# Optimization experiments

Hardware: AMD Instinct MI355X
Metric: run time of the kernel (lower is better)

Reference implementation:

```python
import jax, jax.numpy as jnp
import numpy as np
import math

D_MODEL = 1024
NUM_HEADS = 16
HEAD_DIM = D_MODEL // NUM_HEADS


def setup_inputs() -> dict:
    key = jax.random.key(0)
    ks = jax.random.split(key, 9)
    B, S = 2, 2048
    scale = 1.0 / math.sqrt(D_MODEL)
    x = jax.random.normal(ks[0], (B, S, D_MODEL), dtype=jnp.float32)
    # torch nn.Linear params: weight [out, in], bias [out]
    Wq = jax.random.normal(ks[1], (D_MODEL, D_MODEL), dtype=jnp.float32) * scale
    bq = jax.random.normal(ks[2], (D_MODEL,), dtype=jnp.float32) * scale
    Wk = jax.random.normal(ks[3], (D_MODEL, D_MODEL), dtype=jnp.float32) * scale
    bk = jax.random.normal(ks[4], (D_MODEL,), dtype=jnp.float32) * scale
    Wv = jax.random.normal(ks[5], (D_MODEL, D_MODEL), dtype=jnp.float32) * scale
    bv = jax.random.normal(ks[6], (D_MODEL,), dtype=jnp.float32) * scale
    Wo = jax.random.normal(ks[7], (D_MODEL, D_MODEL), dtype=jnp.float32) * scale
    bo = jax.random.normal(ks[8], (D_MODEL,), dtype=jnp.float32) * scale
    return {"x": x, "Wq": Wq, "bq": bq, "Wk": Wk, "bk": bk,
            "Wv": Wv, "bv": bv, "Wo": Wo, "bo": bo}


def reference(x, Wq, bq, Wk, bk, Wv, bv, Wo, bo):
    B, S, _ = x.shape
    H, Dh = NUM_HEADS, HEAD_DIM

    def proj(W, b):
        # torch Linear: x @ W.T + b -> [B,S,D] -> [B,H,S,Dh]
        y = jnp.einsum('bsd,ed->bse', x, W) + b
        return y.reshape(B, S, H, Dh).transpose(0, 2, 1, 3)

    Q = proj(Wq, bq)
    K = proj(Wk, bk)
    V = proj(Wv, bv)

    # scores [B,H,S,S], causal mask with -inf, then scale by 1/sqrt(head_dim)
    scores = jnp.einsum('bhqd,bhkd->bhqk', Q, K)
    causal = jnp.tril(jnp.ones((S, S), dtype=bool))
    scores = jnp.where(causal, scores, -jnp.inf)
    A = jax.nn.softmax(scores / math.sqrt(Dh), axis=-1)

    O = jnp.einsum('bhqk,bhkd->bhqd', A, V)  # [B,H,S,Dh]
    O = O.transpose(0, 2, 1, 3).reshape(B, S, H * Dh)
    return jnp.einsum('bsd,ed->bse', O, Wo) + bo
```

## Files before the change

### kernel.cpp

```cpp
#include <hip/hip_runtime.h>


typedef _Float16 f16x8 __attribute__((ext_vector_type(8)));
typedef _Float16 f16x4 __attribute__((ext_vector_type(4)));
typedef _Float16 f16x2 __attribute__((ext_vector_type(2)));
typedef float f32x4 __attribute__((ext_vector_type(4)));

#define S_  2048
#define DM  1024
#define NH  16
#define DH  64

__device__ __forceinline__ void gload_lds16(const void* g, void* s) {
  __builtin_amdgcn_global_load_lds(
      (const __attribute__((address_space(1))) void*)g,
      (__attribute__((address_space(3))) void*)s, 16, 0, 0);
}

__device__ __forceinline__ f16x2 pkrtz(float a, float b) {
  return __builtin_bit_cast(f16x2, __builtin_amdgcn_cvt_pkrtz(a, b));
}


__global__ void cvt_all_kernel(const float* __restrict__ x,
                               const float* __restrict__ w0,
                               const float* __restrict__ w1,
                               const float* __restrict__ w2,
                               const float* __restrict__ w3,
                               _Float16* __restrict__ xb,
                               _Float16* __restrict__ wb) {
  const int bid = blockIdx.x;
  const float* src;
  _Float16* dst;
  int idx;
  if (bid < 4096) {
    src = x; dst = xb; idx = bid * 256 + threadIdx.x;
  } else {
    const int j = bid - 4096;
    const int y = j >> 10;
    src = (y == 0) ? w0 : (y == 1) ? w1 : (y == 2) ? w2 : w3;
    dst = wb + (size_t)y * (DM * DM);
    idx = (j & 1023) * 256 + threadIdx.x;
  }
  const float4 v = ((const float4*)src)[idx];
  f16x4 h;
  h[0] = (_Float16)v.x; h[1] = (_Float16)v.y;
  h[2] = (_Float16)v.z; h[3] = (_Float16)v.w;
  ((f16x4*)dst)[idx] = h;
}


__global__ __launch_bounds__(256, 2) void gemm_qkv_kernel(
    const _Float16* __restrict__ xb, const _Float16* __restrict__ wb,
    const float* __restrict__ bq, const float* __restrict__ bk,
    const float* __restrict__ bv, _Float16* __restrict__ qkv)
{
  __shared__ _Float16 As[2][128 * 32];
  __shared__ _Float16 Ws[2][128 * 32];
  const int z = blockIdx.z;
  const _Float16* W = wb + (size_t)z * (DM * DM);
  const float* bias = (z == 0) ? bq : ((z == 1) ? bk : bv);
  _Float16* out = qkv + (size_t)z * 4194304;

  const f32x4 z4 = {0.f, 0.f, 0.f, 0.f};
  f32x4 acc[4][4];
#pragma unroll
  for (int mi = 0; mi < 4; ++mi)
#pragma unroll
    for (int ni = 0; ni < 4; ++ni) acc[mi][ni] = z4;

  const int m0 = blockIdx.y * 128, n0 = blockIdx.x * 128;
  const int t = threadIdx.x;
  const int w = t >> 6, l = t & 63;
  const int quad = l >> 4, ln = l & 15;
  const int wm = (w >> 1) << 6, wn = (w & 1) << 6;
  const int srow = l >> 2, scol = (l & 3) << 3;

  for (int k0 = 0; k0 < DM; k0 += 64) {
#pragma unroll
    for (int h = 0; h < 2; ++h)
#pragma unroll
      for (int i = 0; i < 2; ++i) {
        const int ra = w * 32 + i * 16;
        gload_lds16(&xb[(size_t)(m0 + ra + srow) * DM + k0 + h * 32 + scol],
                    &As[h][ra * 32]);
        gload_lds16(&W[(size_t)(n0 + ra + srow) * DM + k0 + h * 32 + scol],
                    &Ws[h][ra * 32]);
      }
    __syncthreads();

#pragma unroll
    for (int h = 0; h < 2; ++h) {
      f16x8 af[4], bf[4];
#pragma unroll
      for (int mi = 0; mi < 4; ++mi)
        af[mi] = *(const f16x8*)&As[h][(wm + mi * 16 + ln) * 32 + quad * 8];
#pragma unroll
      for (int ni = 0; ni < 4; ++ni)
        bf[ni] = *(const f16x8*)&Ws[h][(wn + ni * 16 + ln) * 32 + quad * 8];
#pragma unroll
      for (int mi = 0; mi < 4; ++mi)
#pragma unroll
        for (int ni = 0; ni < 4; ++ni)
          acc[mi][ni] = __builtin_amdgcn_mfma_f32_16x16x32_f16(
              af[mi], bf[ni], acc[mi][ni], 0, 0, 0);
    }
    __syncthreads();
  }

  const float scale = (z == 0) ? 0.18033688f : 1.0f;

#pragma unroll
  for (int ni = 0; ni < 4; ++ni) {
    const int c = n0 + wn + ni * 16 + ln;
    const float bias_c = bias[c];
    const int h = c >> 6, d = c & 63;
#pragma unroll
    for (int mi = 0; mi < 4; ++mi) {
      const int mb = m0 + wm + mi * 16 + quad * 4;
#pragma unroll
      for (int r = 0; r < 4; ++r) {
        const int mg = mb + r;
        const int b = mg >> 11, s = mg & 2047;
        const int bh = b * NH + h;
        const float v = (acc[mi][ni][r] + bias_c) * scale;
        size_t idx;
        if (z == 2)
          idx = (size_t)bh * 131072 + (s >> 5) * 2048 + (d >> 4) * 512 +
                ((s >> 3) & 3) * 128 + (d & 15) * 8 + (s & 7);
        else
          idx = (size_t)bh * 131072 + (s >> 4) * 1024 + (d >> 5) * 512 +
                ((d >> 3) & 3) * 128 + (s & 15) * 8 + (d & 7);
        out[idx] = (_Float16)v;
      }
    }
  }
}


__global__ __launch_bounds__(256, 2) void gemm_out_kernel(
    const _Float16* __restrict__ ob, const _Float16* __restrict__ wo,
    const float* __restrict__ bo, float* __restrict__ out)
{
  __shared__ _Float16 As[2][128 * 32];
  __shared__ _Float16 Ws[2][64 * 32];
  const f32x4 z4 = {0.f, 0.f, 0.f, 0.f};
  f32x4 acc[2][4];
#pragma unroll
  for (int mi = 0; mi < 2; ++mi)
#pragma unroll
    for (int ni = 0; ni < 4; ++ni) acc[mi][ni] = z4;

  const int m0 = blockIdx.y * 128, n0 = blockIdx.x * 64;
  const int t = threadIdx.x;
  const int w = t >> 6, l = t & 63;
  const int quad = l >> 4, ln = l & 15;
  const int srow = l >> 2, scol = (l & 3) << 3;

  for (int k0 = 0; k0 < DM; k0 += 64) {
#pragma unroll
    for (int h = 0; h < 2; ++h) {
#pragma unroll
      for (int i = 0; i < 2; ++i) {
        const int ra = w * 32 + i * 16;
        gload_lds16(&ob[(size_t)(m0 + ra + srow) * DM + k0 + h * 32 + scol],
                    &As[h][ra * 32]);
      }
      gload_lds16(&wo[(size_t)(n0 + w * 16 + srow) * DM + k0 + h * 32 + scol],
                  &Ws[h][w * 16 * 32]);
    }
    __syncthreads();

#pragma unroll
    for (int h = 0; h < 2; ++h) {
      f16x8 af[2], bf[4];
#pragma unroll
      for (int mi = 0; mi < 2; ++mi)
        af[mi] = *(const f16x8*)&As[h][(w * 32 + mi * 16 + ln) * 32 + quad * 8];
#pragma unroll
      for (int ni = 0; ni < 4; ++ni)
        bf[ni] = *(const f16x8*)&Ws[h][(ni * 16 + ln) * 32 + quad * 8];
#pragma unroll
      for (int mi = 0; mi < 2; ++mi)
#pragma unroll
        for (int ni = 0; ni < 4; ++ni)
          acc[mi][ni] = __builtin_amdgcn_mfma_f32_16x16x32_f16(
              af[mi], bf[ni], acc[mi][ni], 0, 0, 0);
    }
    __syncthreads();
  }

#pragma unroll
  for (int ni = 0; ni < 4; ++ni) {
    const int c = n0 + ni * 16 + ln;
    const float bias_c = bo[c];
#pragma unroll
    for (int mi = 0; mi < 2; ++mi) {
      const int mb = m0 + w * 32 + mi * 16 + quad * 4;
#pragma unroll
      for (int r = 0; r < 4; ++r)
        out[(size_t)(mb + r) * DM + c] = acc[mi][ni][r] + bias_c;
    }
  }
}


template <bool DIAG>
__device__ __forceinline__ void tile16(
    const _Float16* __restrict__ kb_, const _Float16* __restrict__ vb_,
    int t, const f16x8 (&qf)[2], f32x4 (&oacc)[4], float& l_i,
    _Float16* Ps, int quad, int ln, int l, int h)
{
  const f32x4 z4 = {0.f, 0.f, 0.f, 0.f};
  f16x8 kv[4];

#pragma unroll
  for (int ii = 0; ii < 4; ++ii)
    kv[ii] = *(const f16x8*)(kb_ + (size_t)(t * 4 + ii) * 512 + l * 8);

  f32x4 sacc[2];
  sacc[0] = z4; sacc[1] = z4;
#pragma unroll
  for (int ks = 0; ks < 2; ++ks)
#pragma unroll
    for (int mi = 0; mi < 2; ++mi)
      sacc[mi] = __builtin_amdgcn_mfma_f32_16x16x32_f16(
          kv[mi * 2 + ks], qf[ks], sacc[mi], 0, 0, 0);

#pragma unroll
  for (int ii = 0; ii < 4; ++ii)
    kv[ii] = *(const f16x8*)(vb_ + (size_t)(t * 4 + ii) * 512 + l * 8);

  float rs = 0.f;
#pragma unroll
  for (int mi = 0; mi < 2; ++mi) {
    float p[4];
#pragma unroll
    for (int r = 0; r < 4; ++r) {
      p[r] = __builtin_amdgcn_exp2f(sacc[mi][r]);
      if (DIAG && (mi * 16 + quad * 4 + r > h * 16 + ln)) p[r] = 0.f;
      rs += p[r];
    }
    const f16x2 lo = pkrtz(p[0], p[1]);
    const f16x2 hi = pkrtz(p[2], p[3]);
    const f16x4 pk = __builtin_shufflevector(lo, hi, 0, 1, 2, 3);
    const int slot = ((mi * 4 + quad) + 2 * ln) & 15;
    *(f16x4*)&Ps[ln * 64 + slot * 4] = pk;
  }
  l_i += rs;

  const int slot2 = ((quad * 2) + 2 * ln) & 15;
  const f16x8 pb = *(const f16x8*)&Ps[ln * 64 + slot2 * 4];

#pragma unroll
  for (int di = 0; di < 4; ++di)
    oacc[di] = __builtin_amdgcn_mfma_f32_16x16x32_f16(
        kv[di], pb, oacc[di], 0, 0, 0);
}

__global__ __launch_bounds__(256, 6) void attn_kernel(
    const _Float16* __restrict__ QF, const _Float16* __restrict__ KF,
    const _Float16* __restrict__ VF, _Float16* __restrict__ Ob)
{
  __shared__ _Float16 Ps[4 * 16 * 64];
  __shared__ float mrgO[2][1024];
  __shared__ float mrgL[2][64];

  const int i = blockIdx.x;
  const int bh = i & 31;
  const int a = 63 - (i >> 5);

  const int tid = threadIdx.x;
  const int w = tid >> 6, l = tid & 63;
  const int quad = l >> 4, ln = l & 15;
  const int h = w >> 1;
  const int e = w & 1;

  const _Float16* qb_ = QF + (size_t)bh * 131072;
  const _Float16* kb_ = KF + (size_t)bh * 131072;
  const _Float16* vb_ = VF + (size_t)bh * 131072;
  _Float16* psw = Ps + w * (16 * 64);
  const int bidx = bh >> 4, hh = bh & 15;

  f16x8 qf[2];
#pragma unroll
  for (int ks = 0; ks < 2; ++ks)
    qf[ks] = *(const f16x8*)
        (qb_ + (size_t)((a * 2 + h) * 2 + ks) * 512 + l * 8);

  const f32x4 z4 = {0.f, 0.f, 0.f, 0.f};
  f32x4 oacc[4];
#pragma unroll
  for (int di = 0; di < 4; ++di) oacc[di] = z4;
  float l_i = 0.f;

  int t = e;
  for (; t < a; t += 2)
    tile16<false>(kb_, vb_, t, qf, oacc, l_i, psw, quad, ln, l, h);
  if (t == a)
    tile16<true>(kb_, vb_, t, qf, oacc, l_i, psw, quad, ln, l, h);

  if (e) {
#pragma unroll
    for (int di = 0; di < 4; ++di)
      *(f32x4*)&mrgO[h][di * 256 + l * 4] = oacc[di];
    mrgL[h][l] = l_i;
  }
  __syncthreads();
  if (!e) {
#pragma unroll
    for (int di = 0; di < 4; ++di)
      oacc[di] += *(const f32x4*)&mrgO[h][di * 256 + l * 4];
    l_i += mrgL[h][l];
    l_i += __shfl_xor(l_i, 16);
    l_i += __shfl_xor(l_i, 32);
    const float inv = 1.0f / l_i;

    const int q = a * 32 + h * 16 + ln;
    _Float16* orow = Ob + (size_t)(bidx * S_ + q) * DM + hh * DH + quad * 4;
#pragma unroll
    for (int di = 0; di < 4; ++di) {
      f16x4 o4;
#pragma unroll
      for (int r = 0; r < 4; ++r)
        o4[r] = (_Float16)(oacc[di][r] * inv);
      *(f16x4*)(orow + di * 16) = o4;
    }
  }
}


extern "C" void kernel_launch(void* const* d_in, const int* in_sizes, int n_in,
                              void* d_out, int out_size, void* d_ws, size_t ws_size,
                              hipStream_t stream) {
  (void)in_sizes; (void)n_in; (void)out_size; (void)ws_size;
  const float* x  = (const float*)d_in[0];
  const float* Wq = (const float*)d_in[1];
  const float* bq = (const float*)d_in[2];
  const float* Wk = (const float*)d_in[3];
  const float* bk = (const float*)d_in[4];
  const float* Wv = (const float*)d_in[5];
  const float* bv = (const float*)d_in[6];
  const float* Wo = (const float*)d_in[7];
  const float* bo = (const float*)d_in[8];

  char* ws = (char*)d_ws;
  _Float16* xb  = (_Float16*)(ws);
  _Float16* wb  = (_Float16*)(ws + (8u << 20));
  _Float16* qkv = (_Float16*)(ws + (16u << 20));
  _Float16* ob  = (_Float16*)(ws + (40u << 20));

  cvt_all_kernel<<<dim3(8192), dim3(256), 0, stream>>>(x, Wq, Wk, Wv, Wo, xb, wb);
  gemm_qkv_kernel<<<dim3(8, 32, 3), dim3(256), 0, stream>>>(xb, wb, bq, bk, bv, qkv);
  attn_kernel<<<dim3(2048), dim3(256), 0, stream>>>(
      qkv, qkv + 4194304, qkv + 2 * 4194304, ob);
  gemm_out_kernel<<<dim3(16, 32), dim3(256), 0, stream>>>(
      ob, wb + (size_t)3 * DM * DM, bo, (float*)d_out);
}
```

Measured before the change: 183.0 us.

## Share K/V tiles across waves via double-buffered LDS in attention

The attention kernel now gives each block 64 query rows (four waves, 16 rows each) instead of 32 rows split over two key-parity waves. K and V tiles are streamed into double-buffered LDS with global_load_lds and shared by all four waves, replacing per-wave global loads and the cross-wave merge of partial outputs. The grid is halved. This cuts redundant K/V global traffic but adds two barriers per tile, and waves with earlier diagonals sit idle on later tiles.

```diff
diff --git a/kernel.cpp b/kernel.cpp
--- a/kernel.cpp
+++ b/kernel.cpp
@@ -206,17 +206,17 @@
 
 
 template <bool DIAG>
-__device__ __forceinline__ void tile16(
-    const _Float16* __restrict__ kb_, const _Float16* __restrict__ vb_,
-    int t, const f16x8 (&qf)[2], f32x4 (&oacc)[4], float& l_i,
-    _Float16* Ps, int quad, int ln, int l, int h)
+__device__ __forceinline__ void tile_lds(
+    const _Float16* __restrict__ Kls, const _Float16* __restrict__ Vls,
+    const f16x8 (&qf)[2], f32x4 (&oacc)[4], float& l_i,
+    _Float16* Ps, int quad, int ln, int l, int hq)
 {
   const f32x4 z4 = {0.f, 0.f, 0.f, 0.f};
   f16x8 kv[4];
 
 #pragma unroll
   for (int ii = 0; ii < 4; ++ii)
-    kv[ii] = *(const f16x8*)(kb_ + (size_t)(t * 4 + ii) * 512 + l * 8);
+    kv[ii] = *(const f16x8*)&Kls[ii * 512 + l * 8];
 
   f32x4 sacc[2];
   sacc[0] = z4; sacc[1] = z4;
@@ -229,7 +229,7 @@
 
 #pragma unroll
   for (int ii = 0; ii < 4; ++ii)
-    kv[ii] = *(const f16x8*)(vb_ + (size_t)(t * 4 + ii) * 512 + l * 8);
+    kv[ii] = *(const f16x8*)&Vls[ii * 512 + l * 8];
 
   float rs = 0.f;
 #pragma unroll
@@ -238,7 +238,7 @@
 #pragma unroll
     for (int r = 0; r < 4; ++r) {
       p[r] = __builtin_amdgcn_exp2f(sacc[mi][r]);
-      if (DIAG && (mi * 16 + quad * 4 + r > h * 16 + ln)) p[r] = 0.f;
+      if (DIAG && (mi * 16 + quad * 4 + r > hq + ln)) p[r] = 0.f;
       rs += p[r];
     }
     const f16x2 lo = pkrtz(p[0], p[1]);
@@ -262,31 +262,31 @@
     const _Float16* __restrict__ QF, const _Float16* __restrict__ KF,
     const _Float16* __restrict__ VF, _Float16* __restrict__ Ob)
 {
+  __shared__ _Float16 KVs[2][2][2048];
   __shared__ _Float16 Ps[4 * 16 * 64];
-  __shared__ float mrgO[2][1024];
-  __shared__ float mrgL[2][64];
 
   const int i = blockIdx.x;
   const int bh = i & 31;
-  const int a = 63 - (i >> 5);
+  const int b  = 31 - (i >> 5);
+  const int T  = 2 * b + 2;
 
   const int tid = threadIdx.x;
   const int w = tid >> 6, l = tid & 63;
   const int quad = l >> 4, ln = l & 15;
-  const int h = w >> 1;
-  const int e = w & 1;
+  const int hq = (w & 1) << 4;
+  const int Dw = 2 * b + (w >> 1);
 
   const _Float16* qb_ = QF + (size_t)bh * 131072;
   const _Float16* kb_ = KF + (size_t)bh * 131072;
   const _Float16* vb_ = VF + (size_t)bh * 131072;
-  _Float16* psw = Ps + w * (16 * 64);
+  _Float16* psw = Ps + w * 1024;
   const int bidx = bh >> 4, hh = bh & 15;
 
   f16x8 qf[2];
 #pragma unroll
   for (int ks = 0; ks < 2; ++ks)
     qf[ks] = *(const f16x8*)
-        (qb_ + (size_t)((a * 2 + h) * 2 + ks) * 512 + l * 8);
+        (qb_ + (size_t)((4 * b + w) * 2 + ks) * 512 + l * 8);
 
   const f32x4 z4 = {0.f, 0.f, 0.f, 0.f};
   f32x4 oacc[4];
@@ -294,38 +294,45 @@
   for (int di = 0; di < 4; ++di) oacc[di] = z4;
   float l_i = 0.f;
 
-  int t = e;
-  for (; t < a; t += 2)
-    tile16<false>(kb_, vb_, t, qf, oacc, l_i, psw, quad, ln, l, h);
-  if (t == a)
-    tile16<true>(kb_, vb_, t, qf, oacc, l_i, psw, quad, ln, l, h);
-
-  if (e) {
-#pragma unroll
-    for (int di = 0; di < 4; ++di)
-      *(f32x4*)&mrgO[h][di * 256 + l * 4] = oacc[di];
-    mrgL[h][l] = l_i;
-  }
-  __syncthreads();
-  if (!e) {
-#pragma unroll
-    for (int di = 0; di < 4; ++di)
-      oacc[di] += *(const f32x4*)&mrgO[h][di * 256 + l * 4];
-    l_i += mrgL[h][l];
-    l_i += __shfl_xor(l_i, 16);
-    l_i += __shfl_xor(l_i, 32);
-    const float inv = 1.0f / l_i;
-
-    const int q = a * 32 + h * 16 + ln;
-    _Float16* orow = Ob + (size_t)(bidx * S_ + q) * DM + hh * DH + quad * 4;
-#pragma unroll
-    for (int di = 0; di < 4; ++di) {
-      f16x4 o4;
-#pragma unroll
-      for (int r = 0; r < 4; ++r)
-        o4[r] = (_Float16)(oacc[di][r] * inv);
-      *(f16x4*)(orow + di * 16) = o4;
-    }
+  gload_lds16(&kb_[(size_t)w * 512 + l * 8], &KVs[0][0][w * 512]);
+  gload_lds16(&vb_[(size_t)w * 512 + l * 8], &KVs[0][1][w * 512]);
+
+  for (int t = 0; t < T; ++t) {
+    const int cur = t & 1;
+    if (t + 1 < T) {
+      gload_lds16(&kb_[(size_t)(t + 1) * 2048 + w * 512 + l * 8],
+                  &KVs[cur ^ 1][0][w * 512]);
+      gload_lds16(&vb_[(size_t)(t + 1) * 2048 + w * 512 + l * 8],
+                  &KVs[cur ^ 1][1][w * 512]);
+      asm volatile("s_waitcnt vmcnt(2)" ::: "memory");
+    } else {
+      asm volatile("s_waitcnt vmcnt(0)" ::: "memory");
+    }
+    __builtin_amdgcn_s_barrier();
+    __builtin_amdgcn_sched_barrier(0);
+    if (t < Dw)
+      tile_lds<false>(&KVs[cur][0][0], &KVs[cur][1][0], qf, oacc, l_i,
+                      psw, quad, ln, l, hq);
+    else if (t == Dw)
+      tile_lds<true>(&KVs[cur][0][0], &KVs[cur][1][0], qf, oacc, l_i,
+                     psw, quad, ln, l, hq);
+    __builtin_amdgcn_sched_barrier(0);
+    __builtin_amdgcn_s_barrier();
+  }
+
+  l_i += __shfl_xor(l_i, 16);
+  l_i += __shfl_xor(l_i, 32);
+  const float inv = 1.0f / l_i;
+
+  const int q = b * 64 + w * 16 + ln;
+  _Float16* orow = Ob + (size_t)(bidx * S_ + q) * DM + hh * DH + quad * 4;
+#pragma unroll
+  for (int di = 0; di < 4; ++di) {
+    f16x4 o4;
+#pragma unroll
+    for (int r = 0; r < 4; ++r)
+      o4[r] = (_Float16)(oacc[di][r] * inv);
+    *(f16x4*)(orow + di * 16) = o4;
   }
 }
 
@@ -352,7 +359,7 @@
 
   cvt_all_kernel<<<dim3(8192), dim3(256), 0, stream>>>(x, Wq, Wk, Wv, Wo, xb, wb);
   gemm_qkv_kernel<<<dim3(8, 32, 3), dim3(256), 0, stream>>>(xb, wb, bq, bk, bv, qkv);
-  attn_kernel<<<dim3(2048), dim3(256), 0, stream>>>(
+  attn_kernel<<<dim3(1024), dim3(256), 0, stream>>>(
       qkv, qkv + 4194304, qkv + 2 * 4194304, ob);
   gemm_out_kernel<<<dim3(16, 32), dim3(256), 0, stream>>>(
       ob, wb + (size_t)3 * DM * DM, bo, (float*)d_out);
```

Result: no change. 186.3 us (+1.8%).

## Process 64 query rows per attention wave to reuse K/V loads

Applied to the files above, without the earlier changes.

The attention kernel now has each wave handle four 16-row query sub-tiles over a 32-key tile, so every K and V fragment loaded from global memory is reused across 64 query rows instead of 16. Blocks shrink to two waves that split the key tiles and merge their partial sums in shared memory, and the grid halves to 1024 blocks. The diagonal tiles are handled with per-sub-tile masking modes. This cuts redundant K/V traffic but raises register use (launch bounds drop to 3 waves-per-EU hint) and lowers the total wave count, which risks lower occupancy and worse load balance.

```diff
diff --git a/kernel.cpp b/kernel.cpp
--- a/kernel.cpp
+++ b/kernel.cpp
@@ -205,126 +205,142 @@
 }
 
 
-template <bool DIAG>
-__device__ __forceinline__ void tile16(
+template <int MODE>
+__device__ __forceinline__ void tile64(
     const _Float16* __restrict__ kb_, const _Float16* __restrict__ vb_,
-    int t, const f16x8 (&qf)[2], f32x4 (&oacc)[4], float& l_i,
-    _Float16* Ps, int quad, int ln, int l, int h)
+    int t, const f16x8 (&qf)[4][2], f32x4 (&oacc)[4][4], float (&l_i)[4],
+    _Float16* Ps, int quad, int ln, int l)
 {
+  f16x8 kr[4], vr[4];
+#pragma unroll
+  for (int ii = 0; ii < 4; ++ii)
+    kr[ii] = *(const f16x8*)(kb_ + (size_t)t * 2048 + ii * 512 + l * 8);
+#pragma unroll
+  for (int ii = 0; ii < 4; ++ii)
+    vr[ii] = *(const f16x8*)(vb_ + (size_t)t * 2048 + ii * 512 + l * 8);
+
   const f32x4 z4 = {0.f, 0.f, 0.f, 0.f};
-  f16x8 kv[4];
-
-#pragma unroll
-  for (int ii = 0; ii < 4; ++ii)
-    kv[ii] = *(const f16x8*)(kb_ + (size_t)(t * 4 + ii) * 512 + l * 8);
-
-  f32x4 sacc[2];
-  sacc[0] = z4; sacc[1] = z4;
-#pragma unroll
-  for (int ks = 0; ks < 2; ++ks)
-#pragma unroll
-    for (int mi = 0; mi < 2; ++mi)
-      sacc[mi] = __builtin_amdgcn_mfma_f32_16x16x32_f16(
-          kv[mi * 2 + ks], qf[ks], sacc[mi], 0, 0, 0);
-
-#pragma unroll
-  for (int ii = 0; ii < 4; ++ii)
-    kv[ii] = *(const f16x8*)(vb_ + (size_t)(t * 4 + ii) * 512 + l * 8);
-
-  float rs = 0.f;
-#pragma unroll
-  for (int mi = 0; mi < 2; ++mi) {
-    float p[4];
-#pragma unroll
-    for (int r = 0; r < 4; ++r) {
-      p[r] = __builtin_amdgcn_exp2f(sacc[mi][r]);
-      if (DIAG && (mi * 16 + quad * 4 + r > h * 16 + ln)) p[r] = 0.f;
-      rs += p[r];
-    }
-    const f16x2 lo = pkrtz(p[0], p[1]);
-    const f16x2 hi = pkrtz(p[2], p[3]);
-    const f16x4 pk = __builtin_shufflevector(lo, hi, 0, 1, 2, 3);
-    const int slot = ((mi * 4 + quad) + 2 * ln) & 15;
-    *(f16x4*)&Ps[ln * 64 + slot * 4] = pk;
-  }
-  l_i += rs;
-
-  const int slot2 = ((quad * 2) + 2 * ln) & 15;
-  const f16x8 pb = *(const f16x8*)&Ps[ln * 64 + slot2 * 4];
-
-#pragma unroll
-  for (int di = 0; di < 4; ++di)
-    oacc[di] = __builtin_amdgcn_mfma_f32_16x16x32_f16(
-        kv[di], pb, oacc[di], 0, 0, 0);
-}
-
-__global__ __launch_bounds__(256, 6) void attn_kernel(
+#pragma unroll
+  for (int qs = 0; qs < 4; ++qs) {
+    if (MODE == 2 && qs < 2) continue;
+
+    f32x4 sacc[2];
+    sacc[0] = z4; sacc[1] = z4;
+#pragma unroll
+    for (int ks = 0; ks < 2; ++ks)
+#pragma unroll
+      for (int mi = 0; mi < 2; ++mi)
+        sacc[mi] = __builtin_amdgcn_mfma_f32_16x16x32_f16(
+            kr[mi * 2 + ks], qf[qs][ks], sacc[mi], 0, 0, 0);
+
+    const bool DG = (MODE == 1 && qs < 2) || (MODE == 2);
+    const int hq = ((MODE == 1) ? qs : (qs - 2)) << 4;
+
+    float rs = 0.f;
+#pragma unroll
+    for (int mi = 0; mi < 2; ++mi) {
+      float p[4];
+#pragma unroll
+      for (int r = 0; r < 4; ++r) {
+        p[r] = __builtin_amdgcn_exp2f(sacc[mi][r]);
+        if (DG && (mi * 16 + quad * 4 + r > hq + ln)) p[r] = 0.f;
+        rs += p[r];
+      }
+      const f16x2 lo = pkrtz(p[0], p[1]);
+      const f16x2 hi = pkrtz(p[2], p[3]);
+      const f16x4 pk = __builtin_shufflevector(lo, hi, 0, 1, 2, 3);
+      const int slot = ((mi * 4 + quad) + 2 * ln) & 15;
+      *(f16x4*)&Ps[ln * 64 + slot * 4] = pk;
+    }
+    l_i[qs] += rs;
+
+    const int slot2 = ((quad * 2) + 2 * ln) & 15;
+    const f16x8 pb = *(const f16x8*)&Ps[ln * 64 + slot2 * 4];
+
+#pragma unroll
+    for (int di = 0; di < 4; ++di)
+      oacc[qs][di] = __builtin_amdgcn_mfma_f32_16x16x32_f16(
+          vr[di], pb, oacc[qs][di], 0, 0, 0);
+  }
+}
+
+__global__ __launch_bounds__(128, 3) void attn_kernel(
     const _Float16* __restrict__ QF, const _Float16* __restrict__ KF,
     const _Float16* __restrict__ VF, _Float16* __restrict__ Ob)
 {
-  __shared__ _Float16 Ps[4 * 16 * 64];
-  __shared__ float mrgO[2][1024];
-  __shared__ float mrgL[2][64];
+  __shared__ _Float16 Ps[2][1024];
+  __shared__ float mrgO[4][1024];
+  __shared__ float mrgL[4][64];
 
   const int i = blockIdx.x;
   const int bh = i & 31;
-  const int a = 63 - (i >> 5);
+  const int qb = 31 - (i >> 5);
 
   const int tid = threadIdx.x;
-  const int w = tid >> 6, l = tid & 63;
+  const int e = tid >> 6, l = tid & 63;
   const int quad = l >> 4, ln = l & 15;
-  const int h = w >> 1;
-  const int e = w & 1;
 
   const _Float16* qb_ = QF + (size_t)bh * 131072;
   const _Float16* kb_ = KF + (size_t)bh * 131072;
   const _Float16* vb_ = VF + (size_t)bh * 131072;
-  _Float16* psw = Ps + w * (16 * 64);
+  _Float16* psw = &Ps[e][0];
   const int bidx = bh >> 4, hh = bh & 15;
 
-  f16x8 qf[2];
-#pragma unroll
-  for (int ks = 0; ks < 2; ++ks)
-    qf[ks] = *(const f16x8*)
-        (qb_ + (size_t)((a * 2 + h) * 2 + ks) * 512 + l * 8);
+  f16x8 qf[4][2];
+#pragma unroll
+  for (int qs = 0; qs < 4; ++qs)
+#pragma unroll
+    for (int ks = 0; ks < 2; ++ks)
+      qf[qs][ks] = *(const f16x8*)
+          (qb_ + (size_t)((4 * qb + qs) * 2 + ks) * 512 + l * 8);
 
   const f32x4 z4 = {0.f, 0.f, 0.f, 0.f};
-  f32x4 oacc[4];
-#pragma unroll
-  for (int di = 0; di < 4; ++di) oacc[di] = z4;
-  float l_i = 0.f;
+  f32x4 oacc[4][4];
+#pragma unroll
+  for (int qs = 0; qs < 4; ++qs)
+#pragma unroll
+    for (int di = 0; di < 4; ++di) oacc[qs][di] = z4;
+  float l_i[4] = {0.f, 0.f, 0.f, 0.f};
 
   int t = e;
-  for (; t < a; t += 2)
-    tile16<false>(kb_, vb_, t, qf, oacc, l_i, psw, quad, ln, l, h);
-  if (t == a)
-    tile16<true>(kb_, vb_, t, qf, oacc, l_i, psw, quad, ln, l, h);
+  for (; t < 2 * qb; t += 2)
+    tile64<0>(kb_, vb_, t, qf, oacc, l_i, psw, quad, ln, l);
+  if (e == 0)
+    tile64<1>(kb_, vb_, 2 * qb, qf, oacc, l_i, psw, quad, ln, l);
+  else
+    tile64<2>(kb_, vb_, 2 * qb + 1, qf, oacc, l_i, psw, quad, ln, l);
 
   if (e) {
 #pragma unroll
-    for (int di = 0; di < 4; ++di)
-      *(f32x4*)&mrgO[h][di * 256 + l * 4] = oacc[di];
-    mrgL[h][l] = l_i;
+    for (int qs = 0; qs < 4; ++qs) {
+#pragma unroll
+      for (int di = 0; di < 4; ++di)
+        *(f32x4*)&mrgO[qs][di * 256 + l * 4] = oacc[qs][di];
+      mrgL[qs][l] = l_i[qs];
+    }
   }
   __syncthreads();
   if (!e) {
 #pragma unroll
-    for (int di = 0; di < 4; ++di)
-      oacc[di] += *(const f32x4*)&mrgO[h][di * 256 + l * 4];
-    l_i += mrgL[h][l];
-    l_i += __shfl_xor(l_i, 16);
-    l_i += __shfl_xor(l_i, 32);
-    const float inv = 1.0f / l_i;
-
-    const int q = a * 32 + h * 16 + ln;
-    _Float16* orow = Ob + (size_t)(bidx * S_ + q) * DM + hh * DH + quad * 4;
-#pragma unroll
-    for (int di = 0; di < 4; ++di) {
-      f16x4 o4;
-#pragma unroll
-      for (int r = 0; r < 4; ++r)
-        o4[r] = (_Float16)(oacc[di][r] * inv);
-      *(f16x4*)(orow + di * 16) = o4;
+    for (int qs = 0; qs < 4; ++qs) {
+#pragma unroll
+      for (int di = 0; di < 4; ++di)
+        oacc[qs][di] += *(const f32x4*)&mrgO[qs][di * 256 + l * 4];
+      float li = l_i[qs] + mrgL[qs][l];
+      li += __shfl_xor(li, 16);
+      li += __shfl_xor(li, 32);
+      const float inv = 1.0f / li;
+
+      const int q = qb * 64 + qs * 16 + ln;
+      _Float16* orow = Ob + (size_t)(bidx * S_ + q) * DM + hh * DH + quad * 4;
+#pragma unroll
+      for (int di = 0; di < 4; ++di) {
+        f16x4 o4;
+#pragma unroll
+        for (int r = 0; r < 4; ++r)
+          o4[r] = (_Float16)(oacc[qs][di][r] * inv);
+        *(f16x4*)(orow + di * 16) = o4;
+      }
     }
   }
 }
@@ -352,7 +368,7 @@
 
   cvt_all_kernel<<<dim3(8192), dim3(256), 0, stream>>>(x, Wq, Wk, Wv, Wo, xb, wb);
   gemm_qkv_kernel<<<dim3(8, 32, 3), dim3(256), 0, stream>>>(xb, wb, bq, bk, bv, qkv);
-  attn_kernel<<<dim3(2048), dim3(256), 0, stream>>>(
+  attn_kernel<<<dim3(1024), dim3(128), 0, stream>>>(
       qkv, qkv + 4194304, qkv + 2 * 4194304, ob);
   gemm_out_kernel<<<dim3(16, 32), dim3(256), 0, stream>>>(
       ob, wb + (size_t)3 * DM * DM, bo, (float*)d_out);
```

After: 181.8 us. Within noise of the previous version (-0.6%).
